# Kernel tuning notes

Hardware: AMD Instinct MI355X
Metric: run time of the kernel (lower is better)

Reference implementation:

```python
import jax, jax.numpy as jnp
import numpy as np

N, F_IN, F_OUT = 8192, 512, 256


def setup_inputs() -> dict:
    key = jax.random.key(0)
    k1, k2, k3, k4 = jax.random.split(key, 4)
    x = jax.random.normal(k1, (N, F_IN), dtype=jnp.float32)
    adj = jax.random.randint(k2, (N, N), 0, 2, dtype=jnp.int32)
    # xavier_uniform with gain=1.414
    limW = 1.414 * np.sqrt(6.0 / (F_IN + F_OUT))
    W = jax.random.uniform(k3, (F_IN, F_OUT), dtype=jnp.float32, minval=-limW, maxval=limW)
    lima = 1.414 * np.sqrt(6.0 / (2 * F_OUT + 1))
    a = jax.random.uniform(k4, (2 * F_OUT, 1), dtype=jnp.float32, minval=-lima, maxval=lima)
    return {"x": x, "adj": adj, "W": W, "a": a}


def reference(x, adj, W, a):
    # h = x @ W : [N, F_out]
    h = x @ W
    f_out = h.shape[1]
    # additive score a^T [h_i ; h_j] is separable: (h @ a_l)_i + (h @ a_r)_j
    f_src = h @ a[:f_out, 0]   # [N]
    f_dst = h @ a[f_out:, 0]   # [N]
    e = jax.nn.leaky_relu(f_src[:, None] + f_dst[None, :], negative_slope=0.2)  # [N, N]
    e = jnp.where(adj > 0, e, jnp.float32(-9e15))
    attention = jax.nn.softmax(e, axis=1)  # row-wise over neighbors
    # dropout(p=0.6) is identity in eval mode
    h_prime = attention @ h  # [N, F_out]
    return h_prime
```

## Files before the change

kernel.cpp:

```cpp
#include <hip/hip_runtime.h>
#include <hip/hip_bf16.h>

#define NN 8192
#define FIN 512
#define FOUT 256
#define JTILE 64
#define FDWIN 2048

typedef __attribute__((ext_vector_type(8))) short short8;
typedef __attribute__((ext_vector_type(4))) float float4v;
typedef __attribute__((ext_vector_type(4))) int int4v;
typedef __attribute__((ext_vector_type(16))) float float16v;

#if __has_builtin(__builtin_amdgcn_exp2f)
#define EXP2(x) __builtin_amdgcn_exp2f(x)
#else
#define EXP2(x) exp2f(x)
#endif

__device__ __forceinline__ short f2bf(float f) {
    union { float f; unsigned u; } v; v.f = f;
    unsigned r = (v.u + 0x7FFFu + ((v.u >> 16) & 1u)) >> 16;
    return (short)r;
}

__device__ __forceinline__ unsigned cvt_pk_bf16(float lo, float hi) {
    unsigned r;
    asm("v_cvt_pk_bf16_f32 %0, %1, %2" : "=v"(r) : "v"(lo), "v"(hi));
    return r;
}

__global__ __launch_bounds__(256) void wt_kernel(const float* __restrict__ W,
                                                 short* __restrict__ Wt) {
    __shared__ short tile[32][33];
    int tx = threadIdx.x & 31, ty = threadIdx.x >> 5;
    int k0 = blockIdx.x * 32, n0 = blockIdx.y * 32;
#pragma unroll
    for (int r = 0; r < 32; r += 8)
        tile[ty + r][tx] = f2bf(W[(size_t)(k0 + ty + r) * FOUT + n0 + tx]);
    __syncthreads();
#pragma unroll
    for (int r = 0; r < 32; r += 8)
        Wt[(size_t)(n0 + ty + r) * FIN + k0 + tx] = tile[tx][ty + r];
}

__global__ __launch_bounds__(256) void h_kernel(const float* __restrict__ x,
                                                const short* __restrict__ Wt,
                                                const float* __restrict__ a,
                                                short* __restrict__ h_t,
                                                float* __restrict__ f_src,
                                                float* __restrict__ f_dst) {
    int wave = (blockIdx.x << 2) + (threadIdx.x >> 6);
    int lane = threadIdx.x & 63;
    int m0 = (wave & 511) << 4;
    int n0 = (wave >> 9) << 6;
    int lr = lane & 15, lq = lane >> 4;

    const float* xrow = x + (size_t)(m0 + lr) * FIN + lq * 8;
    const short* wbase = Wt + (size_t)(n0 + lr) * FIN + lq * 8;

    float4v acc[4] = {};
    for (int k0 = 0; k0 < FIN; k0 += 32) {
        float4v xa = *(const float4v*)(xrow + k0);
        float4v xb = *(const float4v*)(xrow + k0 + 4);
        short8 av;
        av[0] = f2bf(xa[0]); av[1] = f2bf(xa[1]); av[2] = f2bf(xa[2]); av[3] = f2bf(xa[3]);
        av[4] = f2bf(xb[0]); av[5] = f2bf(xb[1]); av[6] = f2bf(xb[2]); av[7] = f2bf(xb[3]);
#pragma unroll
        for (int ct = 0; ct < 4; ct++) {
            short8 bv = *(const short8*)(wbase + (size_t)ct * 16 * FIN + k0);
            acc[ct] = __builtin_amdgcn_mfma_f32_16x16x32_bf16(av, bv, acc[ct], 0, 0, 0);
        }
    }
    float s_part[4] = {0.f, 0.f, 0.f, 0.f};
    float d_part[4] = {0.f, 0.f, 0.f, 0.f};
#pragma unroll
    for (int ct = 0; ct < 4; ct++) {
        int n = n0 + ct * 16 + lr;
        float al = a[n], ar = a[FOUT + n];
#pragma unroll
        for (int reg = 0; reg < 4; reg++) {
            float hv = acc[ct][reg];
            s_part[reg] = fmaf(hv, al, s_part[reg]);
            d_part[reg] = fmaf(hv, ar, d_part[reg]);
            h_t[(size_t)n * NN + (m0 + lq * 4 + reg)] = f2bf(hv);
        }
    }
#pragma unroll
    for (int off = 1; off < 16; off <<= 1) {
#pragma unroll
        for (int reg = 0; reg < 4; reg++) {
            s_part[reg] += __shfl_xor(s_part[reg], off);
            d_part[reg] += __shfl_xor(d_part[reg], off);
        }
    }
    const float LOG2E = 1.4426950408889634f;
    if (lr == 0) {
#pragma unroll
        for (int reg = 0; reg < 4; reg++) {
            atomicAdd(&f_src[m0 + lq * 4 + reg], s_part[reg] * LOG2E);
            atomicAdd(&f_dst[m0 + lq * 4 + reg], d_part[reg] * LOG2E);
        }
    }
}

__global__ __launch_bounds__(256, 3) void gat_kernel(const int* __restrict__ adj,
                                                     const short* __restrict__ h_t,
                                                     const float* __restrict__ f_src,
                                                     const float* __restrict__ f_dst,
                                                     float* __restrict__ Opart,
                                                     float* __restrict__ lpart,
                                                     int qt, int rt_) {
    __shared__ short Pt[2][64 * 64];
    __shared__ float Fdall[FDWIN];

    const int t = threadIdx.x;
    const int i0 = blockIdx.x * 64;
    const int slice = blockIdx.y;
    const int stile = slice * qt + (slice < rt_ ? slice : rt_);
    const int jbase = stile * 128;
    const int jlen = (qt + (slice < rt_ ? 1 : 0)) * 128;

    const int prow = t >> 2, pjq = t & 3;
    const int lane = t & 63, wv = t >> 6;
    const int l31 = lane & 31, lq = lane >> 5;
    const int wn0 = wv * 64;

    const float fs = f_src[i0 + prow];
    const int* adjRow = adj + (size_t)(i0 + prow) * NN + jbase;
    const short* hb0 = h_t + (size_t)(wn0 + l31) * NN + jbase + lq * 8;
    const short* hb1 = hb0 + (size_t)32 * NN;

    float16v acc00 = {}, acc01 = {}, acc10 = {}, acc11 = {};
    float lp = 0.f;

    const int pswz = (prow & 7) << 4;
    const int rswz = (l31 & 7) << 4;
    const int wb = prow * 128 + pjq * 32;
    const int ra = l31 * 128 + lq * 16;

    int4v av0, av1, av2, av3;

#define PPAIR(AE0, AE1, FI, PKI)                                        \
    {                                                                   \
        float y0 = fs + fdp[FI], y1 = fs + fdp[(FI) + 1];               \
        y0 = fmaxf(y0, 0.2f * y0); y1 = fmaxf(y1, 0.2f * y1);           \
        float p0 = ((AE0) != 0) ? EXP2(y0) : 0.f;                       \
        float p1 = ((AE1) != 0) ? EXP2(y1) : 0.f;                       \
        lp += p0 + p1;                                                  \
        pk[PKI] = cvt_pk_bf16(p0, p1);                                  \
    }

    for (int w0 = 0; w0 < jlen; w0 += FDWIN) {
        const int wl = (jlen - w0 < FDWIN) ? (jlen - w0) : FDWIN;
        if (t * 8 < wl) {
            *(float4v*)&Fdall[t * 8]     = *(const float4v*)(f_dst + jbase + w0 + t * 8);
            *(float4v*)&Fdall[t * 8 + 4] = *(const float4v*)(f_dst + jbase + w0 + t * 8 + 4);
        }
        __syncthreads();
        {
            const int4v* ap_ = (const int4v*)(adjRow + w0 + pjq * 16);
            av0 = __builtin_nontemporal_load(ap_);
            av1 = __builtin_nontemporal_load(ap_ + 1);
            av2 = __builtin_nontemporal_load(ap_ + 2);
            av3 = __builtin_nontemporal_load(ap_ + 3);
        }
        for (int jo = w0; jo < w0 + wl; jo += JTILE) {
            const int buf = (jo >> 6) & 1;
            short8 b0_[4], b1_[4];
#pragma unroll
            for (int kk = 0; kk < 4; kk++) {
                b0_[kk] = *(const short8*)(hb0 + jo + kk * 16);
                b1_[kk] = *(const short8*)(hb1 + jo + kk * 16);
            }
            {
                const float* fdp = &Fdall[jo - w0 + pjq * 16];
                unsigned pk[8];
                PPAIR(av0[0], av0[1], 0, 0)  PPAIR(av0[2], av0[3], 2, 1)
                PPAIR(av1[0], av1[1], 4, 2)  PPAIR(av1[2], av1[3], 6, 3)
                PPAIR(av2[0], av2[1], 8, 4)  PPAIR(av2[2], av2[3], 10, 5)
                PPAIR(av3[0], av3[1], 12, 6) PPAIR(av3[2], av3[3], 14, 7)
                char* pbuf_ = (char*)&Pt[buf][0];
                int4v lov, hiv;
                lov[0] = (int)pk[0]; lov[1] = (int)pk[1]; lov[2] = (int)pk[2]; lov[3] = (int)pk[3];
                hiv[0] = (int)pk[4]; hiv[1] = (int)pk[5]; hiv[2] = (int)pk[6]; hiv[3] = (int)pk[7];
                *(int4v*)(pbuf_ + (wb ^ pswz)) = lov;
                *(int4v*)(pbuf_ + ((wb + 16) ^ pswz)) = hiv;
            }
            {
                const int jn = (jo + JTILE < w0 + wl) ? (jo + JTILE) : w0;
                const int4v* ap_ = (const int4v*)(adjRow + jn + pjq * 16);
                av0 = __builtin_nontemporal_load(ap_);
                av1 = __builtin_nontemporal_load(ap_ + 1);
                av2 = __builtin_nontemporal_load(ap_ + 2);
                av3 = __builtin_nontemporal_load(ap_ + 3);
            }
            asm volatile("s_waitcnt lgkmcnt(0)\n\ts_barrier" ::: "memory");
            __builtin_amdgcn_s_setprio(1);
            {
                const char* pbuf_ = (const char*)&Pt[buf][0];
#pragma unroll
                for (int kk = 0; kk < 4; kk++) {
                    short8 a0_ = *(const short8*)(pbuf_ + ((ra + kk * 32) ^ rswz));
                    short8 a1_ = *(const short8*)(pbuf_ + ((ra + 4096 + kk * 32) ^ rswz));
                    acc00 = __builtin_amdgcn_mfma_f32_32x32x16_bf16(a0_, b0_[kk], acc00, 0, 0, 0);
                    acc01 = __builtin_amdgcn_mfma_f32_32x32x16_bf16(a0_, b1_[kk], acc01, 0, 0, 0);
                    acc10 = __builtin_amdgcn_mfma_f32_32x32x16_bf16(a1_, b0_[kk], acc10, 0, 0, 0);
                    acc11 = __builtin_amdgcn_mfma_f32_32x32x16_bf16(a1_, b1_[kk], acc11, 0, 0, 0);
                }
            }
            __builtin_amdgcn_s_setprio(0);
        }
    }
#undef PPAIR

    lp += __shfl_xor(lp, 1);
    lp += __shfl_xor(lp, 2);
    if (pjq == 0) lpart[slice * NN + i0 + prow] = lp;

    float* obase = Opart + ((size_t)slice * NN + i0) * FOUT;
#pragma unroll
    for (int rt = 0; rt < 2; rt++) {
#pragma unroll
        for (int nt = 0; nt < 2; nt++) {
            const float16v& av = rt == 0 ? (nt == 0 ? acc00 : acc01) : (nt == 0 ? acc10 : acc11);
#pragma unroll
            for (int reg = 0; reg < 16; reg++) {
                int row = rt * 32 + (reg & 3) + 8 * (reg >> 2) + 4 * lq;
                int n = wn0 + nt * 32 + l31;
                obase[(size_t)row * FOUT + n] = av[reg];
            }
        }
    }
}

__global__ __launch_bounds__(256) void combine_kernel(const float* __restrict__ Opart,
                                                      const float* __restrict__ lpart,
                                                      float* __restrict__ out, int slices) {
    int i = blockIdx.x, n = threadIdx.x;
    float o = 0.f, l = 0.f;
    for (int s = 0; s < slices; s++) {
        o += Opart[((size_t)s * NN + i) * FOUT + n];
        l += lpart[s * NN + i];
    }
    out[(size_t)i * FOUT + n] = o / l;
}

extern "C" void kernel_launch(void* const* d_in, const int* in_sizes, int n_in,
                              void* d_out, int out_size, void* d_ws, size_t ws_size,
                              hipStream_t stream) {
    const float* x   = (const float*)d_in[0];
    const int*   adj = (const int*)d_in[1];
    const float* W   = (const float*)d_in[2];
    const float* a   = (const float*)d_in[3];
    float* out = (float*)d_out;

    char* ws = (char*)d_ws;
    short* h_t   = (short*)ws;
    short* Wt    = (short*)(ws + (4u << 20));
    float* f_src = (float*)(ws + (4u << 20) + (256u << 10));
    float* f_dst = (float*)(ws + (4u << 20) + (288u << 10));
    float* lpart = (float*)(ws + (4u << 20) + (320u << 10));
    float* Opart = (float*)(ws + (5u << 20));

    const size_t OSLICE = (size_t)NN * FOUT * 4;
    int slices = 1;
    if (ws_size >= (size_t)(5u << 20) + 6 * OSLICE) slices = 6;
    else if (ws_size >= (size_t)(5u << 20) + 4 * OSLICE) slices = 4;
    else if (ws_size >= (size_t)(5u << 20) + 2 * OSLICE) slices = 2;
    const int NTILES = NN / 128;
    int qt = NTILES / slices, rt_ = NTILES % slices;

    hipMemsetAsync(f_src, 0, 2 * NN * sizeof(float), stream);
    wt_kernel<<<dim3(FIN / 32, FOUT / 32), 256, 0, stream>>>(W, Wt);
    h_kernel<<<512, 256, 0, stream>>>(x, Wt, a, h_t, f_src, f_dst);
    gat_kernel<<<dim3(NN / 64, slices), 256, 0, stream>>>(adj, h_t, f_src, f_dst,
                                                          Opart, lpart, qt, rt_);
    combine_kernel<<<NN, 256, 0, stream>>>(Opart, lpart, out, slices);
}
```

Before: 476.3 us.

## Pack adjacency into a bitmask in a fused pre-pass and read bits in attention

Result: slower. 558.0 us (+17.2%).

```diff
diff --git a/kernel.cpp b/kernel.cpp
--- a/kernel.cpp
+++ b/kernel.cpp
@@ -6,6 +6,7 @@
 #define FOUT 256
 #define JTILE 64
 #define FDWIN 2048
+#define NWRD (NN / 32)
 
 typedef __attribute__((ext_vector_type(8))) short short8;
 typedef __attribute__((ext_vector_type(4))) float float4v;
@@ -44,12 +45,33 @@
         Wt[(size_t)(n0 + ty + r) * FIN + k0 + tx] = tile[tx][ty + r];
 }
 
-__global__ __launch_bounds__(256) void h_kernel(const float* __restrict__ x,
-                                                const short* __restrict__ Wt,
-                                                const float* __restrict__ a,
-                                                short* __restrict__ h_t,
-                                                float* __restrict__ f_src,
-                                                float* __restrict__ f_dst) {
+__global__ __launch_bounds__(256) void hm_kernel(const float* __restrict__ x,
+                                                 const short* __restrict__ Wt,
+                                                 const float* __restrict__ a,
+                                                 const int* __restrict__ adj,
+                                                 short* __restrict__ h_t,
+                                                 float* __restrict__ f_src,
+                                                 float* __restrict__ f_dst,
+                                                 unsigned* __restrict__ mask) {
+    if (blockIdx.x >= 512) {
+        const int mb = blockIdx.x - 512;
+        size_t w = (size_t)mb * 1024 + threadIdx.x;
+#pragma unroll
+        for (int it = 0; it < 4; it++, w += 256) {
+            const int4v* p = (const int4v*)(adj + (w << 5));
+            unsigned m = 0;
+#pragma unroll
+            for (int g = 0; g < 8; g++) {
+                int4v v = __builtin_nontemporal_load(p + g);
+                m |= (v[0] != 0 ? 1u : 0u) << (g * 4);
+                m |= (v[1] != 0 ? 1u : 0u) << (g * 4 + 1);
+                m |= (v[2] != 0 ? 1u : 0u) << (g * 4 + 2);
+                m |= (v[3] != 0 ? 1u : 0u) << (g * 4 + 3);
+            }
+            mask[w] = m;
+        }
+        return;
+    }
     int wave = (blockIdx.x << 2) + (threadIdx.x >> 6);
     int lane = threadIdx.x & 63;
     int m0 = (wave & 511) << 4;
@@ -104,7 +126,7 @@
     }
 }
 
-__global__ __launch_bounds__(256, 3) void gat_kernel(const int* __restrict__ adj,
+__global__ __launch_bounds__(256, 3) void gat_kernel(const unsigned* __restrict__ mask,
                                                      const short* __restrict__ h_t,
                                                      const float* __restrict__ f_src,
                                                      const float* __restrict__ f_dst,
@@ -127,7 +149,7 @@
     const int wn0 = wv * 64;
 
     const float fs = f_src[i0 + prow];
-    const int* adjRow = adj + (size_t)(i0 + prow) * NN + jbase;
+    const unsigned* maskRow = mask + (size_t)(i0 + prow) * NWRD + (jbase >> 5);
     const short* hb0 = h_t + (size_t)(wn0 + l31) * NN + jbase + lq * 8;
     const short* hb1 = hb0 + (size_t)32 * NN;
 
@@ -138,15 +160,17 @@
     const int rswz = (l31 & 7) << 4;
     const int wb = prow * 128 + pjq * 32;
     const int ra = l31 * 128 + lq * 16;
-
-    int4v av0, av1, av2, av3;
-
-#define PPAIR(AE0, AE1, FI, PKI)                                        \
+    const int mshift = (pjq & 1) << 4;
+    const int mword = pjq >> 1;
+
+    unsigned mwCur, mwNext;
+
+#define PPAIR(B0, B1, FI, PKI)                                          \
     {                                                                   \
         float y0 = fs + fdp[FI], y1 = fs + fdp[(FI) + 1];               \
         y0 = fmaxf(y0, 0.2f * y0); y1 = fmaxf(y1, 0.2f * y1);           \
-        float p0 = ((AE0) != 0) ? EXP2(y0) : 0.f;                       \
-        float p1 = ((AE1) != 0) ? EXP2(y1) : 0.f;                       \
+        float p0 = (B0) ? EXP2(y0) : 0.f;                               \
+        float p1 = (B1) ? EXP2(y1) : 0.f;                               \
         lp += p0 + p1;                                                  \
         pk[PKI] = cvt_pk_bf16(p0, p1);                                  \
     }
@@ -158,13 +182,8 @@
             *(float4v*)&Fdall[t * 8 + 4] = *(const float4v*)(f_dst + jbase + w0 + t * 8 + 4);
         }
         __syncthreads();
-        {
-            const int4v* ap_ = (const int4v*)(adjRow + w0 + pjq * 16);
-            av0 = __builtin_nontemporal_load(ap_);
-            av1 = __builtin_nontemporal_load(ap_ + 1);
-            av2 = __builtin_nontemporal_load(ap_ + 2);
-            av3 = __builtin_nontemporal_load(ap_ + 3);
-        }
+        mwCur = maskRow[(w0 >> 5) + mword];
+
         for (int jo = w0; jo < w0 + wl; jo += JTILE) {
             const int buf = (jo >> 6) & 1;
             short8 b0_[4], b1_[4];
@@ -174,26 +193,27 @@
                 b1_[kk] = *(const short8*)(hb1 + jo + kk * 16);
             }
             {
+                const int jn = (jo + JTILE < w0 + wl) ? (jo + JTILE) : w0;
+                mwNext = maskRow[(jn >> 5) + mword];
+            }
+            {
                 const float* fdp = &Fdall[jo - w0 + pjq * 16];
+                const unsigned sm = mwCur >> mshift;
                 unsigned pk[8];
-                PPAIR(av0[0], av0[1], 0, 0)  PPAIR(av0[2], av0[3], 2, 1)
-                PPAIR(av1[0], av1[1], 4, 2)  PPAIR(av1[2], av1[3], 6, 3)
-                PPAIR(av2[0], av2[1], 8, 4)  PPAIR(av2[2], av2[3], 10, 5)
-                PPAIR(av3[0], av3[1], 12, 6) PPAIR(av3[2], av3[3], 14, 7)
+                PPAIR((sm >> 0) & 1u,  (sm >> 1) & 1u,  0, 0)
+                PPAIR((sm >> 2) & 1u,  (sm >> 3) & 1u,  2, 1)
+                PPAIR((sm >> 4) & 1u,  (sm >> 5) & 1u,  4, 2)
+                PPAIR((sm >> 6) & 1u,  (sm >> 7) & 1u,  6, 3)
+                PPAIR((sm >> 8) & 1u,  (sm >> 9) & 1u,  8, 4)
+                PPAIR((sm >> 10) & 1u, (sm >> 11) & 1u, 10, 5)
+                PPAIR((sm >> 12) & 1u, (sm >> 13) & 1u, 12, 6)
+                PPAIR((sm >> 14) & 1u, (sm >> 15) & 1u, 14, 7)
                 char* pbuf_ = (char*)&Pt[buf][0];
                 int4v lov, hiv;
                 lov[0] = (int)pk[0]; lov[1] = (int)pk[1]; lov[2] = (int)pk[2]; lov[3] = (int)pk[3];
                 hiv[0] = (int)pk[4]; hiv[1] = (int)pk[5]; hiv[2] = (int)pk[6]; hiv[3] = (int)pk[7];
                 *(int4v*)(pbuf_ + (wb ^ pswz)) = lov;
                 *(int4v*)(pbuf_ + ((wb + 16) ^ pswz)) = hiv;
-            }
-            {
-                const int jn = (jo + JTILE < w0 + wl) ? (jo + JTILE) : w0;
-                const int4v* ap_ = (const int4v*)(adjRow + jn + pjq * 16);
-                av0 = __builtin_nontemporal_load(ap_);
-                av1 = __builtin_nontemporal_load(ap_ + 1);
-                av2 = __builtin_nontemporal_load(ap_ + 2);
-                av3 = __builtin_nontemporal_load(ap_ + 3);
             }
             asm volatile("s_waitcnt lgkmcnt(0)\n\ts_barrier" ::: "memory");
             __builtin_amdgcn_s_setprio(1);
@@ -210,6 +230,7 @@
                 }
             }
             __builtin_amdgcn_s_setprio(0);
+            mwCur = mwNext;
         }
     }
 #undef PPAIR
@@ -264,17 +285,19 @@
     float* Opart = (float*)(ws + (5u << 20));
 
     const size_t OSLICE = (size_t)NN * FOUT * 4;
+    const size_t MASKSZ = (size_t)NN * NN / 8;
     int slices = 1;
-    if (ws_size >= (size_t)(5u << 20) + 6 * OSLICE) slices = 6;
-    else if (ws_size >= (size_t)(5u << 20) + 4 * OSLICE) slices = 4;
-    else if (ws_size >= (size_t)(5u << 20) + 2 * OSLICE) slices = 2;
+    if (ws_size >= (size_t)(5u << 20) + 6 * OSLICE + MASKSZ) slices = 6;
+    else if (ws_size >= (size_t)(5u << 20) + 4 * OSLICE + MASKSZ) slices = 4;
+    else if (ws_size >= (size_t)(5u << 20) + 2 * OSLICE + MASKSZ) slices = 2;
+    unsigned* mask = (unsigned*)(ws + (5u << 20) + (size_t)slices * OSLICE);
     const int NTILES = NN / 128;
     int qt = NTILES / slices, rt_ = NTILES % slices;
 
     hipMemsetAsync(f_src, 0, 2 * NN * sizeof(float), stream);
     wt_kernel<<<dim3(FIN / 32, FOUT / 32), 256, 0, stream>>>(W, Wt);
-    h_kernel<<<512, 256, 0, stream>>>(x, Wt, a, h_t, f_src, f_dst);
-    gat_kernel<<<dim3(NN / 64, slices), 256, 0, stream>>>(adj, h_t, f_src, f_dst,
+    hm_kernel<<<2560, 256, 0, stream>>>(x, Wt, a, adj, h_t, f_src, f_dst, mask);
+    gat_kernel<<<dim3(NN / 64, slices), 256, 0, stream>>>(mask, h_t, f_src, f_dst,
                                                           Opart, lpart, qt, rt_);
     combine_kernel<<<NN, 256, 0, stream>>>(Opart, lpart, out, slices);
 }
```
